# Performance work log

Hardware: AMD Instinct MI355X
Metric: run time of the kernel (lower is better)

The kernel has to match this reference:

```python
import jax, jax.numpy as jnp
import numpy as np

B, L, S, H, E = 2, 2048, 2048, 16, 64


def setup_inputs() -> dict:
    key = jax.random.key(0)
    kq, kk, kv = jax.random.split(key, 3)
    queries = jax.random.normal(kq, (B, L, H, E), dtype=jnp.float32)
    keys = jax.random.normal(kk, (B, S, H, E), dtype=jnp.float32)
    values = jax.random.normal(kv, (B, S, H, E), dtype=jnp.float32)
    attn_mask = jnp.ones((B, 1, L, S), dtype=jnp.float32)  # >0.5 means attend
    return {"queries": queries, "keys": keys, "values": values, "attn_mask": attn_mask}


def reference(queries, keys, values, attn_mask):
    # queries: [B,L,H,E], keys/values: [B,S,H,E], attn_mask broadcastable to [B,H,L,S]
    E_ = queries.shape[-1]
    scale = 1.0 / np.sqrt(E_).astype(np.float32)
    scores = jnp.einsum('blhe,bshe->bhls', queries, keys)  # [B,H,L,S]
    large_negative = jnp.float32(-1e9)
    scores = scores + jnp.where(attn_mask > 0.5, jnp.float32(0.0), large_negative)
    A = jax.nn.softmax(scale * scores, axis=-1)  # dropout p=0.0 -> identity
    V = jnp.einsum('bhls,bshd->bhld', A, values)  # [B,H,L,D]
    return V
```

## Files before the change

kernel.cpp:

```cpp
#include <hip/hip_runtime.h>

typedef float    f32x4 __attribute__((ext_vector_type(4)));
typedef _Float16 f16x2 __attribute__((ext_vector_type(2)));
typedef _Float16 f16x4 __attribute__((ext_vector_type(4)));
typedef _Float16 f16x8 __attribute__((ext_vector_type(8)));
typedef int      i32x4 __attribute__((ext_vector_type(4)));

namespace {
constexpr int B_ = 2, L_ = 2048, S_ = 2048, H_ = 16, E_ = 64;
constexpr int MBLK = 128;
constexpr int NT = 64;
constexpr int NTILES = S_ / NT;

#define SCALE2f 0.1803368801111204f
#define MBIAS2f -1.8033688e8f

constexpr size_t KHOFF = (size_t)1 << 20;
constexpr size_t VHOFF = KHOFF + (size_t)B_ * H_ * S_ * E_ * 2;

__device__ __forceinline__ f16x2 cvt2(float a, float b) {
  return __builtin_bit_cast(f16x2, __builtin_amdgcn_cvt_pkrtz(a, b));
}
__device__ __forceinline__ int pkh(float a, float b) {
  return __builtin_bit_cast(int, __builtin_amdgcn_cvt_pkrtz(a, b));
}
union H8 { f16x8 v; i32x4 i; };
union H4 { f16x4 v; f16x2 h[2]; };

#define GLOAD_LDS16(g, l)                                              \
  __builtin_amdgcn_global_load_lds(                                    \
      (const __attribute__((address_space(1))) void*)(g),              \
      (__attribute__((address_space(3))) void*)(l), 16, 0, 0)
}

extern "C" __global__ __launch_bounds__(256)
void maskpack_kernel(const float* __restrict__ Mg, unsigned long long* __restrict__ Wb) {
  const int w    = (int)((blockIdx.x * 256 + threadIdx.x) >> 6);
  const int lane = threadIdx.x & 63;
  const float* src = Mg + (size_t)w * 2048 + lane;
  unsigned long long* dst = Wb + (size_t)w * 32;
#pragma unroll 8
  for (int j = 0; j < 32; ++j) {
    const unsigned long long bits = __ballot(src[j * 64] > 0.5f);
    if (lane == 0) dst[j] = bits;
  }
}

extern "C" __global__ __launch_bounds__(256)
void kcvt_kernel(const float* __restrict__ Kg, _Float16* __restrict__ Kh) {
  const int idx = blockIdx.x * 256 + threadIdx.x;
  const int j = idx & 7;
  const int h = (idx >> 3) & (H_ - 1);
  const int s = (idx >> 7) & (S_ - 1);
  const int b = idx >> 18;
  const float* src = Kg + ((((size_t)b * S_ + s) * H_ + h) << 6) + j * 8;
  f32x4 x = *(const f32x4*)src, y = *(const f32x4*)(src + 4);
  i32x4 w = {pkh(x[0], x[1]), pkh(x[2], x[3]), pkh(y[0], y[1]), pkh(y[2], y[3])};
  *(i32x4*)(Kh + ((((size_t)b * H_ + h) * S_ + s) << 6) + j * 8) = w;
}

extern "C" __global__ __launch_bounds__(256)
void vcvt_kernel(const float* __restrict__ Vg, _Float16* __restrict__ Vh) {
  __shared__ _Float16 T[64][72];
  const int bid = blockIdx.x;
  const int st = bid & 31;
  const int h  = (bid >> 5) & (H_ - 1);
  const int b  = bid >> 9;
  const int t  = threadIdx.x;
  const int sl = t >> 2;
  const int e0 = (t & 3) << 4;
  const float* src = Vg + ((((size_t)b * S_ + st * 64 + sl) * H_ + h) << 6) + e0;
#pragma unroll
  for (int i = 0; i < 4; ++i) {
    f32x4 x = *(const f32x4*)(src + i * 4);
#pragma unroll
    for (int c = 0; c < 4; ++c) T[e0 + i * 4 + c][sl] = (_Float16)x[c];
  }
  __syncthreads();
  const int er = t >> 2;
  const int s0 = (t & 3) << 4;
  _Float16* dst = Vh + (((((size_t)b * H_ + h) << 6) + er) * S_) + st * 64 + s0;
  *(i32x4*)dst       = *(const i32x4*)&T[er][s0];
  *(i32x4*)(dst + 8) = *(const i32x4*)&T[er][s0 + 8];
}

extern "C" __global__ __launch_bounds__(256, 2)
void fattn_kernel(const float* __restrict__ Qg, const _Float16* __restrict__ Kh,
                  const _Float16* __restrict__ Vh, const unsigned long long* __restrict__ Wb,
                  float* __restrict__ Og) {
  __shared__ __align__(16) _Float16 Ks[2][NT][64];
  __shared__ __align__(16) _Float16 Vt[2][E_][64];

  const int tid  = threadIdx.x;
  const int wv   = tid >> 6;
  const int lane = tid & 63;
  const int qd   = lane >> 4;
  const int cl   = lane & 15;
  const int sw   = cl & 7;

  const int bid = blockIdx.x;
  const int qb  = bid >> 5;
  const int bh  = bid & 31;
  const int h   = bh & (H_ - 1);
  const int b   = bh >> 4;

  const int l0 = qb * MBLK + wv * 32;

  f16x8 qf[2][2];
#pragma unroll
  for (int mt = 0; mt < 2; ++mt) {
    const float* qp = Qg + ((((size_t)b * L_ + (l0 + mt * 16 + cl)) * H_ + h) << 6);
#pragma unroll
    for (int kb = 0; kb < 2; ++kb) {
      const int e0 = qd * 8 + kb * 32;
      f32x4 x = *(const f32x4*)(qp + e0);
      f32x4 y = *(const f32x4*)(qp + e0 + 4);
      H8 u;
      u.i = (i32x4){pkh(x[0], x[1]), pkh(x[2], x[3]), pkh(y[0], y[1]), pkh(y[2], y[3])};
      qf[mt][kb] = u.v;
    }
  }

  const int rl  = lane >> 3;
  const int gsl = lane & 7;
  const int gsw = gsl ^ rl;
  const _Float16* khb = Kh + ((((size_t)b * H_ + h) * S_) << 6);
  const _Float16* vhb = Vh + ((((size_t)b * H_ + h) << 6) * (size_t)S_);

  const unsigned long long* wbp = Wb + (((size_t)b * L_ + (l0 + cl)) << 5);

  auto dma = [&](int buf, int t) {
#pragma unroll
    for (int p = 0; p < 2; ++p) {
      const int r0 = p * 32 + wv * 8;
      const _Float16* ksrc = khb + (((size_t)(t * 64 + r0 + rl)) << 6) + gsw * 8;
      GLOAD_LDS16(ksrc, &Ks[buf][r0][0]);
      const _Float16* vsrc = vhb + (size_t)(r0 + rl) * S_ + t * 64 + gsw * 8;
      GLOAD_LDS16(vsrc, &Vt[buf][r0][0]);
    }
  };

  const f32x4 zero4 = {0.f, 0.f, 0.f, 0.f};
  f32x4 acc[2][4];
#pragma unroll
  for (int mt = 0; mt < 2; ++mt)
#pragma unroll
    for (int et = 0; et < 4; ++et) acc[mt][et] = zero4;
  f32x4 rs4[2] = {zero4, zero4};

  dma(0, 0);
  unsigned long long mwcur = wbp[0];

  for (int t = 0; t < NTILES; ++t) {
    const int cb = t & 1;
    __syncthreads();

    if (t + 1 < NTILES) dma(cb ^ 1, t + 1);
    unsigned long long mwnext = 0;
    if (t + 1 < NTILES) mwnext = wbp[t + 1];

    f32x4 sc[4][2];
#pragma unroll
    for (int nt = 0; nt < 4; ++nt) {
      const _Float16* krow = &Ks[cb][nt * 16 + cl][0];
      const f16x8 a0 = *(const f16x8*)(krow + ((qd ^ sw) << 3));
      const f16x8 a1 = *(const f16x8*)(krow + (((qd + 4) ^ sw) << 3));
#pragma unroll
      for (int mt = 0; mt < 2; ++mt) {
        f32x4 c = zero4;
        c = __builtin_amdgcn_mfma_f32_16x16x32_f16(a0, qf[mt][0], c, 0, 0, 0);
        c = __builtin_amdgcn_mfma_f32_16x16x32_f16(a1, qf[mt][1], c, 0, 0, 0);
        sc[nt][mt] = c;
      }
    }

    f16x4 pa[2][4];
    if (mwcur == ~0ull) {
#pragma unroll
      for (int mt = 0; mt < 2; ++mt)
#pragma unroll
        for (int nt = 0; nt < 4; ++nt) {
          f32x4 p;
#pragma unroll
          for (int r = 0; r < 4; ++r)
            p[r] = __builtin_amdgcn_exp2f(sc[nt][mt][r] * SCALE2f);
          rs4[mt] += p;
          H4 u;
          u.h[0] = cvt2(p[0], p[1]);
          u.h[1] = cvt2(p[2], p[3]);
          pa[mt][nt] = u.v;
        }
    } else {
      const unsigned lo = (unsigned)mwcur;
      const unsigned hi = (unsigned)(mwcur >> 32);
#pragma unroll
      for (int mt = 0; mt < 2; ++mt)
#pragma unroll
        for (int nt = 0; nt < 4; ++nt) {
          const unsigned shm = ((nt < 2) ? lo : hi) >> ((nt & 1) * 16 + qd * 4);
          f32x4 p;
#pragma unroll
          for (int r = 0; r < 4; ++r) {
            const float bias = (shm & (1u << r)) ? 0.f : MBIAS2f;
            p[r] = __builtin_amdgcn_exp2f(__builtin_fmaf(sc[nt][mt][r], SCALE2f, bias));
          }
          rs4[mt] += p;
          H4 u;
          u.h[0] = cvt2(p[0], p[1]);
          u.h[1] = cvt2(p[2], p[3]);
          pa[mt][nt] = u.v;
        }
    }

#pragma unroll
    for (int nt = 0; nt < 4; ++nt)
#pragma unroll
      for (int et = 0; et < 4; ++et) {
        const _Float16* vrow = &Vt[cb][et * 16 + cl][0];
        const f16x4 bv = *(const f16x4*)(vrow + ((((2 * nt + (qd >> 1)) ^ sw) << 3) + ((qd & 1) << 2)));
        acc[0][et] = __builtin_amdgcn_mfma_f32_16x16x16f16(pa[0][nt], bv, acc[0][et], 0, 0, 0);
        acc[1][et] = __builtin_amdgcn_mfma_f32_16x16x16f16(pa[1][nt], bv, acc[1][et], 0, 0, 0);
      }

    mwcur = mwnext;
  }

#pragma unroll
  for (int mt = 0; mt < 2; ++mt) {
    float v = rs4[mt][0] + rs4[mt][1] + rs4[mt][2] + rs4[mt][3];
    v += __shfl_xor(v, 16, 64);
    v += __shfl_xor(v, 32, 64);
#pragma unroll
    for (int r = 0; r < 4; ++r) {
      const float invq = 1.0f / __shfl(v, qd * 4 + r, 64);
      const int l = l0 + mt * 16 + qd * 4 + r;
      float* op = Og + ((((size_t)b * H_ + h) * L_ + l) << 6) + cl;
#pragma unroll
      for (int et = 0; et < 4; ++et) op[et * 16] = acc[mt][et][r] * invq;
    }
  }
}

extern "C" void kernel_launch(void* const* d_in, const int* in_sizes, int n_in,
                              void* d_out, int out_size, void* d_ws, size_t ws_size,
                              hipStream_t stream) {
  const float* Q = (const float*)d_in[0];
  const float* K = (const float*)d_in[1];
  const float* V = (const float*)d_in[2];
  const float* M = (const float*)d_in[3];
  float* O = (float*)d_out;
  unsigned long long* Wb = (unsigned long long*)d_ws;
  _Float16* Khp = (_Float16*)((char*)d_ws + KHOFF);
  _Float16* Vhp = (_Float16*)((char*)d_ws + VHOFF);

  hipLaunchKernelGGL(maskpack_kernel, dim3(B_ * L_ / 4), dim3(256), 0, stream, M, Wb);
  hipLaunchKernelGGL(kcvt_kernel, dim3(B_ * S_ * H_ * 8 / 256), dim3(256), 0, stream, K, Khp);
  hipLaunchKernelGGL(vcvt_kernel, dim3(B_ * H_ * (S_ / 64)), dim3(256), 0, stream, V, Vhp);
  hipLaunchKernelGGL(fattn_kernel, dim3(B_ * H_ * (L_ / MBLK)), dim3(256), 0, stream,
                     Q, Khp, Vhp, Wb, O);
}
```

Before: 175.8 us.

## Software-pipeline QK and PV across tiles and merge prep kernels into one launch

Restructures the attention loop so that the QK^T MFMAs for tile t are issued together with the PV MFMAs for tile t-1. This gives the scheduler independent work to interleave with the exp/softmax step. V gets a third LDS buffer, since the PV for a tile now runs one iteration after its load. The mask-pack, K-convert and V-convert kernels are also merged into a single launch that branches on block index, saving two launch overheads. The costs are more LDS and register pressure, plus a heavier, branchy prep kernel.

```diff
diff --git a/kernel.cpp b/kernel.cpp
--- a/kernel.cpp
+++ b/kernel.cpp
@@ -34,54 +34,53 @@
 }
 
 extern "C" __global__ __launch_bounds__(256)
-void maskpack_kernel(const float* __restrict__ Mg, unsigned long long* __restrict__ Wb) {
-  const int w    = (int)((blockIdx.x * 256 + threadIdx.x) >> 6);
-  const int lane = threadIdx.x & 63;
-  const float* src = Mg + (size_t)w * 2048 + lane;
-  unsigned long long* dst = Wb + (size_t)w * 32;
-#pragma unroll 8
-  for (int j = 0; j < 32; ++j) {
-    const unsigned long long bits = __ballot(src[j * 64] > 0.5f);
-    if (lane == 0) dst[j] = bits;
-  }
-}
-
-extern "C" __global__ __launch_bounds__(256)
-void kcvt_kernel(const float* __restrict__ Kg, _Float16* __restrict__ Kh) {
-  const int idx = blockIdx.x * 256 + threadIdx.x;
-  const int j = idx & 7;
-  const int h = (idx >> 3) & (H_ - 1);
-  const int s = (idx >> 7) & (S_ - 1);
-  const int b = idx >> 18;
-  const float* src = Kg + ((((size_t)b * S_ + s) * H_ + h) << 6) + j * 8;
-  f32x4 x = *(const f32x4*)src, y = *(const f32x4*)(src + 4);
-  i32x4 w = {pkh(x[0], x[1]), pkh(x[2], x[3]), pkh(y[0], y[1]), pkh(y[2], y[3])};
-  *(i32x4*)(Kh + ((((size_t)b * H_ + h) * S_ + s) << 6) + j * 8) = w;
-}
-
-extern "C" __global__ __launch_bounds__(256)
-void vcvt_kernel(const float* __restrict__ Vg, _Float16* __restrict__ Vh) {
+void prep_kernel(const float* __restrict__ Mg, const float* __restrict__ Kg,
+                 const float* __restrict__ Vg, unsigned long long* __restrict__ Wb,
+                 _Float16* __restrict__ Kh, _Float16* __restrict__ Vh) {
   __shared__ _Float16 T[64][72];
   const int bid = blockIdx.x;
-  const int st = bid & 31;
-  const int h  = (bid >> 5) & (H_ - 1);
-  const int b  = bid >> 9;
-  const int t  = threadIdx.x;
-  const int sl = t >> 2;
-  const int e0 = (t & 3) << 4;
-  const float* src = Vg + ((((size_t)b * S_ + st * 64 + sl) * H_ + h) << 6) + e0;
-#pragma unroll
-  for (int i = 0; i < 4; ++i) {
-    f32x4 x = *(const f32x4*)(src + i * 4);
-#pragma unroll
-    for (int c = 0; c < 4; ++c) T[e0 + i * 4 + c][sl] = (_Float16)x[c];
-  }
-  __syncthreads();
-  const int er = t >> 2;
-  const int s0 = (t & 3) << 4;
-  _Float16* dst = Vh + (((((size_t)b * H_ + h) << 6) + er) * S_) + st * 64 + s0;
-  *(i32x4*)dst       = *(const i32x4*)&T[er][s0];
-  *(i32x4*)(dst + 8) = *(const i32x4*)&T[er][s0 + 8];
+  const int tid = threadIdx.x;
+  if (bid < 1024) {
+    const int w    = (bid * 256 + tid) >> 6;
+    const int lane = tid & 63;
+    const float* src = Mg + (size_t)w * 2048 + lane;
+    unsigned long long* dst = Wb + (size_t)w * 32;
+#pragma unroll 8
+    for (int j = 0; j < 32; ++j) {
+      const unsigned long long bits = __ballot(src[j * 64] > 0.5f);
+      if (lane == 0) dst[j] = bits;
+    }
+  } else if (bid < 3072) {
+    const int idx = (bid - 1024) * 256 + tid;
+    const int j = idx & 7;
+    const int h = (idx >> 3) & (H_ - 1);
+    const int s = (idx >> 7) & (S_ - 1);
+    const int b = idx >> 18;
+    const float* src = Kg + ((((size_t)b * S_ + s) * H_ + h) << 6) + j * 8;
+    f32x4 x = *(const f32x4*)src, y = *(const f32x4*)(src + 4);
+    i32x4 w = {pkh(x[0], x[1]), pkh(x[2], x[3]), pkh(y[0], y[1]), pkh(y[2], y[3])};
+    *(i32x4*)(Kh + ((((size_t)b * H_ + h) * S_ + s) << 6) + j * 8) = w;
+  } else {
+    const int vb = bid - 3072;
+    const int st = vb & 31;
+    const int h  = (vb >> 5) & (H_ - 1);
+    const int b  = vb >> 9;
+    const int sl = tid >> 2;
+    const int e0 = (tid & 3) << 4;
+    const float* src = Vg + ((((size_t)b * S_ + st * 64 + sl) * H_ + h) << 6) + e0;
+#pragma unroll
+    for (int i = 0; i < 4; ++i) {
+      f32x4 x = *(const f32x4*)(src + i * 4);
+#pragma unroll
+      for (int c = 0; c < 4; ++c) T[e0 + i * 4 + c][sl] = (_Float16)x[c];
+    }
+    __syncthreads();
+    const int er = tid >> 2;
+    const int s0 = (tid & 3) << 4;
+    _Float16* dst = Vh + (((((size_t)b * H_ + h) << 6) + er) * S_) + st * 64 + s0;
+    *(i32x4*)dst       = *(const i32x4*)&T[er][s0];
+    *(i32x4*)(dst + 8) = *(const i32x4*)&T[er][s0 + 8];
+  }
 }
 
 extern "C" __global__ __launch_bounds__(256, 2)
@@ -89,7 +88,7 @@
                   const _Float16* __restrict__ Vh, const unsigned long long* __restrict__ Wb,
                   float* __restrict__ Og) {
   __shared__ __align__(16) _Float16 Ks[2][NT][64];
-  __shared__ __align__(16) _Float16 Vt[2][E_][64];
+  __shared__ __align__(16) _Float16 Vt[3][E_][64];
 
   const int tid  = threadIdx.x;
   const int wv   = tid >> 6;
@@ -129,14 +128,14 @@
 
   const unsigned long long* wbp = Wb + (((size_t)b * L_ + (l0 + cl)) << 5);
 
-  auto dma = [&](int buf, int t) {
+  auto dma = [&](int kbuf, int vbuf, int t) {
 #pragma unroll
     for (int p = 0; p < 2; ++p) {
       const int r0 = p * 32 + wv * 8;
       const _Float16* ksrc = khb + (((size_t)(t * 64 + r0 + rl)) << 6) + gsw * 8;
-      GLOAD_LDS16(ksrc, &Ks[buf][r0][0]);
+      GLOAD_LDS16(ksrc, &Ks[kbuf][r0][0]);
       const _Float16* vsrc = vhb + (size_t)(r0 + rl) * S_ + t * 64 + gsw * 8;
-      GLOAD_LDS16(vsrc, &Vt[buf][r0][0]);
+      GLOAD_LDS16(vsrc, &Vt[vbuf][r0][0]);
     }
   };
 
@@ -148,21 +147,10 @@
     for (int et = 0; et < 4; ++et) acc[mt][et] = zero4;
   f32x4 rs4[2] = {zero4, zero4};
 
-  dma(0, 0);
-  unsigned long long mwcur = wbp[0];
-
-  for (int t = 0; t < NTILES; ++t) {
-    const int cb = t & 1;
-    __syncthreads();
-
-    if (t + 1 < NTILES) dma(cb ^ 1, t + 1);
-    unsigned long long mwnext = 0;
-    if (t + 1 < NTILES) mwnext = wbp[t + 1];
-
-    f32x4 sc[4][2];
+  auto qk = [&](int kbuf, f32x4 sc[4][2]) {
 #pragma unroll
     for (int nt = 0; nt < 4; ++nt) {
-      const _Float16* krow = &Ks[cb][nt * 16 + cl][0];
+      const _Float16* krow = &Ks[kbuf][nt * 16 + cl][0];
       const f16x8 a0 = *(const f16x8*)(krow + ((qd ^ sw) << 3));
       const f16x8 a1 = *(const f16x8*)(krow + (((qd + 4) ^ sw) << 3));
 #pragma unroll
@@ -173,9 +161,10 @@
         sc[nt][mt] = c;
       }
     }
-
-    f16x4 pa[2][4];
-    if (mwcur == ~0ull) {
+  };
+
+  auto softmax = [&](unsigned long long w, f32x4 sc[4][2], f16x4 pa[2][4]) {
+    if (w == ~0ull) {
 #pragma unroll
       for (int mt = 0; mt < 2; ++mt)
 #pragma unroll
@@ -191,8 +180,8 @@
           pa[mt][nt] = u.v;
         }
     } else {
-      const unsigned lo = (unsigned)mwcur;
-      const unsigned hi = (unsigned)(mwcur >> 32);
+      const unsigned lo = (unsigned)w;
+      const unsigned hi = (unsigned)(w >> 32);
 #pragma unroll
       for (int mt = 0; mt < 2; ++mt)
 #pragma unroll
@@ -211,19 +200,49 @@
           pa[mt][nt] = u.v;
         }
     }
-
+  };
+
+  auto pv = [&](int vbuf, f16x4 pa[2][4]) {
 #pragma unroll
     for (int nt = 0; nt < 4; ++nt)
 #pragma unroll
       for (int et = 0; et < 4; ++et) {
-        const _Float16* vrow = &Vt[cb][et * 16 + cl][0];
+        const _Float16* vrow = &Vt[vbuf][et * 16 + cl][0];
         const f16x4 bv = *(const f16x4*)(vrow + ((((2 * nt + (qd >> 1)) ^ sw) << 3) + ((qd & 1) << 2)));
         acc[0][et] = __builtin_amdgcn_mfma_f32_16x16x16f16(pa[0][nt], bv, acc[0][et], 0, 0, 0);
         acc[1][et] = __builtin_amdgcn_mfma_f32_16x16x16f16(pa[1][nt], bv, acc[1][et], 0, 0, 0);
       }
+  };
+
+  f16x4 pa[2][4];
+  dma(0, 0, 0);
+  unsigned long long mwcur = wbp[0];
+  __syncthreads();
+  dma(1, 1, 1);
+  {
+    f32x4 sc[4][2];
+    qk(0, sc);
+    softmax(mwcur, sc, pa);
+  }
+  mwcur = wbp[1];
+
+  int vr = 0;
+  int vw = 2;
+  for (int t = 1; t < NTILES; ++t) {
+    __syncthreads();
+    if (t + 1 < NTILES) dma((t + 1) & 1, vw, t + 1);
+    const unsigned long long mwnext = (t + 1 < NTILES) ? wbp[t + 1] : 0;
+
+    f32x4 sc[4][2];
+    qk(t & 1, sc);
+    pv(vr, pa);
+    softmax(mwcur, sc, pa);
 
     mwcur = mwnext;
-  }
+    vr = (vr == 2) ? 0 : vr + 1;
+    vw = (vw == 2) ? 0 : vw + 1;
+  }
+  pv(vr, pa);
 
 #pragma unroll
   for (int mt = 0; mt < 2; ++mt) {
@@ -253,9 +272,7 @@
   _Float16* Khp = (_Float16*)((char*)d_ws + KHOFF);
   _Float16* Vhp = (_Float16*)((char*)d_ws + VHOFF);
 
-  hipLaunchKernelGGL(maskpack_kernel, dim3(B_ * L_ / 4), dim3(256), 0, stream, M, Wb);
-  hipLaunchKernelGGL(kcvt_kernel, dim3(B_ * S_ * H_ * 8 / 256), dim3(256), 0, stream, K, Khp);
-  hipLaunchKernelGGL(vcvt_kernel, dim3(B_ * H_ * (S_ / 64)), dim3(256), 0, stream, V, Vhp);
+  hipLaunchKernelGGL(prep_kernel, dim3(4096), dim3(256), 0, stream, M, K, V, Wb, Khp, Vhp);
   hipLaunchKernelGGL(fattn_kernel, dim3(B_ * H_ * (L_ / MBLK)), dim3(256), 0, stream,
                      Q, Khp, Vhp, Wb, O);
 }
```

Measured after the change: 181.1 us. +3.0%, slower.
